# Optimization experiments

Measured on AMD Instinct MI355X. Metric: run time of the kernel, lower is better.

Reference implementation:

```python
import jax, jax.numpy as jnp
import numpy as np

D_MODEL = 2048
N_HEADS = 8
HEAD_DIM = D_MODEL // N_HEADS
SCALING = HEAD_DIM ** -0.5


def setup_inputs() -> dict:
    key = jax.random.key(0)
    ks = jax.random.split(key, 9)
    B, S, D = 2, 2048, D_MODEL
    std = D ** -0.5
    inp = {"x": jax.random.normal(ks[0], (B, S, D), dtype=jnp.float32)}
    names = ["Wq", "Wk", "Wv", "Wo"]
    for i, n in enumerate(names):
        inp[n] = jax.random.normal(ks[1 + i], (D, D), dtype=jnp.float32) * std
        inp["b" + n[1]] = jax.random.normal(ks[5 + i], (D,), dtype=jnp.float32) * 0.01
    return inp


def reference(x, Wq, bq, Wk, bk, Wv, bv, Wo, bo):
    B, S, D = x.shape
    H, hd = N_HEADS, HEAD_DIM

    def proj(W, b):
        # nn.Linear: x @ W.T + b, then split heads -> [B, H, S, hd]
        y = jnp.einsum("bsd,ed->bse", x, W) + b
        return y.reshape(B, S, H, hd).transpose(0, 2, 1, 3)

    q = proj(Wq, bq)
    k = proj(Wk, bk)
    v = proj(Wv, bv)

    # scaled QK^T: [B, H, S, S]
    attn_weights = jnp.einsum("bhqd,bhkd->bhqk", q, k) * SCALING
    causal = jnp.tril(jnp.ones((S, S), dtype=bool))  # [S, S]
    attn_weights = jnp.where(causal[None, None], attn_weights, -jnp.inf)
    attn_probs = jax.nn.softmax(attn_weights, axis=-1)

    out = jnp.einsum("bhqk,bhkd->bhqd", attn_probs, v)  # [B, H, S, hd]
    out = out.transpose(0, 2, 1, 3).reshape(B, S, D)
    out = jnp.einsum("bsd,ed->bse", out, Wo) + bo
    return (out, attn_probs)
```

## Files before the change

### kernel.cpp

```cpp
#include <hip/hip_runtime.h>
#include <cstdint>
#include <cstddef>

typedef _Float16 f16;
typedef __attribute__((ext_vector_type(4))) _Float16 f16x4;
typedef __attribute__((ext_vector_type(8))) _Float16 f16x8;
typedef __attribute__((ext_vector_type(4))) float f32x4;

#define NB 2
#define SEQ 2048
#define DM 2048
#define NH 8
#define HD 256
#define MT (NB * SEQ)

#define QSCALE 0.09016844f
#define CEXP   23.08312065f

__device__ __forceinline__ void gload16(const f16* g, f16* l) {
    __builtin_amdgcn_global_load_lds(
        (const __attribute__((address_space(1))) uint32_t*)(const void*)g,
        (__attribute__((address_space(3))) uint32_t*)(void*)l,
        16, 0, 0);
}

__global__ __launch_bounds__(256) void k_cvt5(
    const float* __restrict__ x, const float* __restrict__ Wq,
    const float* __restrict__ Wk, const float* __restrict__ Wv,
    const float* __restrict__ Wo,
    f16* __restrict__ xh, f16* __restrict__ Wqh, f16* __restrict__ Wkh,
    f16* __restrict__ Wvh, f16* __restrict__ Woh) {
    const int total = (MT * DM + 4 * DM * DM) / 4;
    for (int q = blockIdx.x * blockDim.x + threadIdx.x; q < total;
         q += gridDim.x * blockDim.x) {
        int i = q * 4;
        const float* src; f16* dst; int off;
        if (i < MT * DM) { src = x; dst = xh; off = i; }
        else {
            int j = i - MT * DM;
            int w = j >> 22;
            off = j & ((1 << 22) - 1);
            src = (w == 0) ? Wq : (w == 1) ? Wk : (w == 2) ? Wv : Wo;
            dst = (w == 0) ? Wqh : (w == 1) ? Wkh : (w == 2) ? Wvh : Woh;
        }
        f32x4 v = *(const f32x4*)(src + off);
        f16x4 h;
        h[0] = (f16)v[0]; h[1] = (f16)v[1]; h[2] = (f16)v[2]; h[3] = (f16)v[3];
        *(f16x4*)(dst + off) = h;
    }
}

__device__ __forceinline__ void stage3(const f16* __restrict__ A,
                                       const f16* __restrict__ B,
                                       int m0, int n0, int k0,
                                       f16* AL, f16* BL, int tid, int half) {
#pragma unroll
    for (int jj = 0; jj < 2; ++jj) {
        int j = half * 2 + jj;
        int flat = j * 4096 + tid * 8;
        int r = flat >> 6, c = flat & 63;
        int cs = c ^ ((r & 7) << 3);
        gload16(A + (size_t)(m0 + r) * DM + k0 + cs,
                AL + j * 4096 + (tid >> 6) * 512);
    }
    {
        int j = half;
        int flat = j * 4096 + tid * 8;
        int r = flat >> 6, c = flat & 63;
        int cs = c ^ ((r & 7) << 3);
        gload16(B + (size_t)(n0 + r) * DM + k0 + cs,
                BL + j * 4096 + (tid >> 6) * 512);
    }
}

__device__ __forceinline__ f16x8 rdfrag(const f16* buf, int rowbase, int lr,
                                        int lg, int kk) {
    int row = rowbase + lr;
    int c = (kk * 32 + lg * 8) ^ ((lr & 7) << 3);
    return *(const f16x8*)&buf[row * 64 + c];
}

__device__ __forceinline__ void gemm256x128_core(const f16* __restrict__ A,
                                                 const f16* __restrict__ B,
                                                 int m0, int n0,
                                                 f16* AL, f16* BL,
                                                 f32x4 acc[4][4]) {
    const int tid = threadIdx.x, wave = tid >> 6, lane = tid & 63;
    const int wm = wave >> 1, wn = wave & 1;
    const int lr = lane & 15, lg = lane >> 4;
    const int nt = DM / 64;

    stage3(A, B, m0, n0, 0, AL, BL, tid, 0);
    stage3(A, B, m0, n0, 0, AL, BL, tid, 1);
    stage3(A, B, m0, n0, 64, AL + 16384, BL + 8192, tid, 0);
    stage3(A, B, m0, n0, 64, AL + 16384, BL + 8192, tid, 1);
    asm volatile("s_waitcnt vmcnt(6)" ::: "memory");
    __builtin_amdgcn_s_barrier();
    __builtin_amdgcn_sched_barrier(0);

    for (int kt = 0; kt < nt; ++kt) {
        const f16* Ab = AL + (kt % 3) * 16384;
        const f16* Bb = BL + (kt % 3) * 8192;
        const int arb = wm * 64, brb = wn * 64;

#pragma unroll
        for (int ph = 0; ph < 2; ++ph) {
            f16x8 af[4], bf[4];
#pragma unroll
            for (int mf = 0; mf < 4; ++mf)
                af[mf] = rdfrag(Ab, arb + mf * 16, lr, lg, ph);
#pragma unroll
            for (int nf = 0; nf < 4; ++nf)
                bf[nf] = rdfrag(Bb, brb + nf * 16, lr, lg, ph);

            if (kt + 2 < nt)
                stage3(A, B, m0, n0, (kt + 2) * 64,
                       AL + ((kt + 2) % 3) * 16384,
                       BL + ((kt + 2) % 3) * 8192, tid, ph);

            __builtin_amdgcn_sched_barrier(0);
            if (ph == 1) {
                if (kt + 2 < nt)
                    asm volatile("s_waitcnt vmcnt(6)" ::: "memory");
                else if (kt + 1 < nt)
                    asm volatile("s_waitcnt vmcnt(0)" ::: "memory");
            }
            __builtin_amdgcn_s_barrier();
            asm volatile("s_waitcnt lgkmcnt(0)" ::: "memory");
            __builtin_amdgcn_sched_barrier(0);

            __builtin_amdgcn_s_setprio(1);
#pragma unroll
            for (int mi = 0; mi < 4; ++mi)
#pragma unroll
                for (int nj = 0; nj < 4; ++nj)
                    acc[mi][nj] = __builtin_amdgcn_mfma_f32_16x16x32_f16(
                        af[mi], bf[nj], acc[mi][nj], 0, 0, 0);
            __builtin_amdgcn_s_setprio(0);
            __builtin_amdgcn_s_barrier();
        }
    }
}

__global__ __launch_bounds__(512, 1) void k_proj_qkv(
    const f16* __restrict__ xh, const f16* __restrict__ Wq,
    const f16* __restrict__ Wk, const f16* __restrict__ Wv,
    const float* __restrict__ bq, const float* __restrict__ bk,
    const float* __restrict__ bv,
    f16* __restrict__ Qh, f16* __restrict__ Kh, f16* __restrict__ Vth) {
    __shared__ __align__(16) f16 AL[3 * 16384];
    __shared__ __align__(16) f16 BL[3 * 8192];
    const int mode = blockIdx.z;
    const f16* W = (mode == 0) ? Wq : (mode == 1) ? Wk : Wv;
    const float* bias = (mode == 0) ? bq : (mode == 1) ? bk : bv;

    const int phys = blockIdx.x + 16 * blockIdx.y;
    const int xcdq = phys & 7, idx = phys >> 3;
    const int m0 = (xcdq * 2 + (idx >> 4)) * 256;
    const int n0 = (idx & 15) * 128;

    f32x4 acc[4][4];
#pragma unroll
    for (int mi = 0; mi < 4; ++mi)
#pragma unroll
        for (int nj = 0; nj < 4; ++nj) acc[mi][nj] = (f32x4){0.f, 0.f, 0.f, 0.f};

    gemm256x128_core(xh, W, m0, n0, AL, BL, acc);

    const int lane = threadIdx.x & 63, wave = threadIdx.x >> 6;
    const int wm = wave >> 1, wn = wave & 1;
    const int lr = lane & 15, lg = lane >> 4;
#pragma unroll
    for (int nj = 0; nj < 4; ++nj) {
        int n = n0 + wn * 64 + nj * 16 + lr;
        float bb = bias[n];
        int h = n >> 8, d = n & 255;
#pragma unroll
        for (int mi = 0; mi < 4; ++mi) {
#pragma unroll
            for (int i = 0; i < 4; ++i) {
                int m = m0 + wm * 64 + mi * 16 + lg * 4 + i;
                int b = m >> 11, s = m & 2047;
                float v = acc[mi][nj][i] + bb;
                size_t bh = (size_t)(b * NH + h);
                if (mode == 0)
                    Qh[((bh * SEQ + s) << 8) + d] = (f16)(v * QSCALE);
                else if (mode == 1)
                    Kh[((bh * SEQ + s) << 8) + d] = (f16)v;
                else
                    Vth[((bh * HD + d) << 11) + s] = (f16)v;
            }
        }
    }
}

__global__ __launch_bounds__(512, 1) void k_proj_o(
    const f16* __restrict__ Oh, const f16* __restrict__ Wo,
    const float* __restrict__ bo, float* __restrict__ out) {
    __shared__ __align__(16) f16 AL[3 * 16384];
    __shared__ __align__(16) f16 BL[3 * 8192];

    const int phys = blockIdx.x + 16 * blockIdx.y;
    const int xcdq = phys & 7, idx = phys >> 3;
    const int m0 = (xcdq * 2 + (idx >> 4)) * 256;
    const int n0 = (idx & 15) * 128;

    f32x4 acc[4][4];
#pragma unroll
    for (int mi = 0; mi < 4; ++mi)
#pragma unroll
        for (int nj = 0; nj < 4; ++nj) acc[mi][nj] = (f32x4){0.f, 0.f, 0.f, 0.f};

    gemm256x128_core(Oh, Wo, m0, n0, AL, BL, acc);

    const int lane = threadIdx.x & 63, wave = threadIdx.x >> 6;
    const int wm = wave >> 1, wn = wave & 1;
    const int lr = lane & 15, lg = lane >> 4;
#pragma unroll
    for (int nj = 0; nj < 4; ++nj) {
        int n = n0 + wn * 64 + nj * 16 + lr;
        float bb = bo[n];
#pragma unroll
        for (int mi = 0; mi < 4; ++mi) {
#pragma unroll
            for (int i = 0; i < 4; ++i) {
                int m = m0 + wm * 64 + mi * 16 + lg * 4 + i;
                out[(size_t)m * DM + n] = acc[mi][nj][i] + bb;
            }
        }
    }
}

__device__ __forceinline__ void stageK(const f16* __restrict__ Kb, int kt,
                                       f16* buf, int wave, int lane) {
#pragma unroll
    for (int j = 0; j < 8; ++j) {
        int base = (j * 4 + wave) << 9;
        int flat = base + (lane << 3);
        int r = flat >> 8;
        int c = (flat & 255) ^ ((r & 7) << 3);
        gload16(Kb + (size_t)(kt * 64 + r) * HD + c, buf + base);
    }
}
__device__ __forceinline__ void stageV(const f16* __restrict__ Vb, int kt,
                                       f16* buf, int wave, int lane) {
#pragma unroll
    for (int j = 0; j < 8; ++j) {
        int base = (j * 4 + wave) << 9;
        int flat = base + (lane << 3);
        int rv = flat >> 6;
        int cv = (flat & 63) ^ ((rv & 3) << 3);
        gload16(Vb + ((size_t)rv << 11) + kt * 64 + cv, buf + base);
    }
}

__global__ __launch_bounds__(256, 2) void k_attn(
    const f16* __restrict__ Qh, const f16* __restrict__ Kh,
    const f16* __restrict__ Vth, float* __restrict__ P,
    f16* __restrict__ Oh) {
    __shared__ __align__(16) f16 B0[64 * 256];
    __shared__ __align__(16) f16 B1[64 * 256];
    __shared__ __align__(16) f16 Ps[4][16][72];

    const int bid = blockIdx.x;
    const int xcd = bid & 7;
    const int slot = bid >> 3;
    const int psel = slot >> 5;
    const int s5 = slot & 31;
    const int qb = psel ? s5 : (31 - s5);
    const int bhid = xcd * 2 + psel;
    const int b = bhid >> 3, h = bhid & 7;

    const int q0 = qb * 64;
    const int tid = threadIdx.x, wave = tid >> 6, lane = tid & 63;
    const int lr = lane & 15, lg = lane >> 4;
    const size_t bh = (size_t)bhid;
    const f16* Qb = Qh + (bh << 19);
    const f16* Kb = Kh + (bh << 19);
    const f16* Vb = Vth + (bh << 19);
    float* Pb = P + (bh << 22);

    const int kswz = (lr & 7) << 3;
    const int vswz = (lr & 3) << 3;

    f16x8 aq[8];
    {
        const f16* qrow = Qb + (size_t)(q0 + wave * 16 + lr) * HD + lg * 8;
#pragma unroll
        for (int kk = 0; kk < 8; ++kk) aq[kk] = *(const f16x8*)(qrow + kk * 32);
    }

    const int rowb = q0 + wave * 16 + lg * 4;
    const int nt = qb + 1;

    float psum[4] = {0.f, 0.f, 0.f, 0.f};

    stageK(Kb, 0, B0, wave, lane);
    for (int kt = 0; kt < nt; ++kt) {
        f16* cur = (kt & 1) ? B1 : B0;
        f16* nxt = (kt & 1) ? B0 : B1;
        if (kt + 1 < nt) {
            stageK(Kb, kt + 1, nxt, wave, lane);
            asm volatile("s_waitcnt vmcnt(8)" ::: "memory");
        } else {
            asm volatile("s_waitcnt vmcnt(0)" ::: "memory");
        }
        __builtin_amdgcn_s_barrier();
        __builtin_amdgcn_sched_barrier(0);

        f32x4 s[4];
#pragma unroll
        for (int nj = 0; nj < 4; ++nj) s[nj] = (f32x4){0.f, 0.f, 0.f, 0.f};
        __builtin_amdgcn_s_setprio(1);
#pragma unroll
        for (int kk = 0; kk < 8; ++kk) {
#pragma unroll
            for (int nj = 0; nj < 4; ++nj) {
                f16x8 bk = *(const f16x8*)&cur[(nj * 16 + lr) * 256 +
                                               ((kk * 32 + lg * 8) ^ kswz)];
                s[nj] = __builtin_amdgcn_mfma_f32_16x16x32_f16(aq[kk], bk, s[nj], 0, 0, 0);
            }
        }
        __builtin_amdgcn_s_setprio(0);
        const int colb = kt * 64 + lr;
#pragma unroll
        for (int i = 0; i < 4; ++i) {
            int row = rowb + i;
#pragma unroll
            for (int nj = 0; nj < 4; ++nj)
                psum[i] += (colb + nj * 16 <= row) ? exp2f(s[nj][i] - CEXP) : 0.f;
        }
        asm volatile("" ::: "memory");
        __builtin_amdgcn_s_barrier();
        __builtin_amdgcn_sched_barrier(0);
    }

    float inv[4];
#pragma unroll
    for (int i = 0; i < 4; ++i) {
        float l = psum[i];
        l += __shfl_xor(l, 1);
        l += __shfl_xor(l, 2);
        l += __shfl_xor(l, 4);
        l += __shfl_xor(l, 8);
        inv[i] = 1.f / l;
    }

    f32x4 o[16];
#pragma unroll
    for (int n = 0; n < 16; ++n) o[n] = (f32x4){0.f, 0.f, 0.f, 0.f};

    stageK(Kb, 0, B0, wave, lane);
    for (int kt = 0; kt < nt; ++kt) {
        stageV(Vb, kt, B1, wave, lane);
        if (kt == 0) asm volatile("s_waitcnt vmcnt(8)" ::: "memory");
        else         asm volatile("s_waitcnt vmcnt(10)" ::: "memory");
        __builtin_amdgcn_s_barrier();
        __builtin_amdgcn_sched_barrier(0);

        f32x4 s[4];
#pragma unroll
        for (int nj = 0; nj < 4; ++nj) s[nj] = (f32x4){0.f, 0.f, 0.f, 0.f};
        __builtin_amdgcn_s_setprio(1);
#pragma unroll
        for (int kk = 0; kk < 8; ++kk) {
#pragma unroll
            for (int nj = 0; nj < 4; ++nj) {
                f16x8 bk = *(const f16x8*)&B0[(nj * 16 + lr) * 256 +
                                              ((kk * 32 + lg * 8) ^ kswz)];
                s[nj] = __builtin_amdgcn_mfma_f32_16x16x32_f16(aq[kk], bk, s[nj], 0, 0, 0);
            }
        }
        __builtin_amdgcn_s_setprio(0);
#pragma unroll
        for (int i = 0; i < 4; ++i) {
            int row = rowb + i;
#pragma unroll
            for (int nj = 0; nj < 4; ++nj) {
                int col = kt * 64 + nj * 16 + lr;
                float pv = (col <= row) ? exp2f(s[nj][i] - CEXP) * inv[i] : 0.f;
                Ps[wave][lg * 4 + i][nj * 16 + lr] = (f16)pv;
            }
        }
        asm volatile("s_waitcnt vmcnt(0)" ::: "memory");
        __builtin_amdgcn_s_barrier();
        __builtin_amdgcn_sched_barrier(0);

        if (kt + 1 < nt) stageK(Kb, kt + 1, B0, wave, lane);

        __builtin_amdgcn_s_setprio(1);
#pragma unroll
        for (int kk2 = 0; kk2 < 2; ++kk2) {
            f16x8 pa = *(const f16x8*)&Ps[wave][lr][kk2 * 32 + lg * 8];
#pragma unroll
            for (int n = 0; n < 16; ++n) {
                f16x8 bv = *(const f16x8*)&B1[(n * 16 + lr) * 64 +
                                              ((kk2 * 32 + lg * 8) ^ vswz)];
                o[n] = __builtin_amdgcn_mfma_f32_16x16x32_f16(pa, bv, o[n], 0, 0, 0);
            }
        }
        __builtin_amdgcn_s_setprio(0);

#pragma unroll
        for (int h2 = 0; h2 < 2; ++h2) {
            int rr = h2 * 8 + (lane >> 3);
            int cc = (lane & 7) * 8;
            f16x8 ph = *(const f16x8*)&Ps[wave][rr][cc];
            int row = q0 + wave * 16 + rr;
            float* dst = Pb + (size_t)row * SEQ + kt * 64 + cc;
            f32x4 lo = {(float)ph[0], (float)ph[1], (float)ph[2], (float)ph[3]};
            f32x4 hi = {(float)ph[4], (float)ph[5], (float)ph[6], (float)ph[7]};
            *(f32x4*)dst = lo;
            *(f32x4*)(dst + 4) = hi;
        }

        asm volatile("" ::: "memory");
        __builtin_amdgcn_s_barrier();
        __builtin_amdgcn_sched_barrier(0);
    }

    int kstart = (qb + 1) * 64;
    if (kstart < SEQ) {
        f32x4 z = (f32x4){0.f, 0.f, 0.f, 0.f};
        for (int r = 0; r < 64; ++r) {
            float* rp = Pb + (size_t)(q0 + r) * SEQ;
            for (int c = kstart + tid * 4; c < SEQ; c += 1024)
                *(f32x4*)(rp + c) = z;
        }
    }

#pragma unroll
    for (int n = 0; n < 16; ++n) {
#pragma unroll
        for (int i = 0; i < 4; ++i) {
            int row = rowb + i;
            int d = n * 16 + lr;
            Oh[((size_t)b * SEQ + row) * DM + h * HD + d] = (f16)o[n][i];
        }
    }
}

extern "C" void kernel_launch(void* const* d_in, const int* in_sizes, int n_in,
                              void* d_out, int out_size, void* d_ws, size_t ws_size,
                              hipStream_t stream) {
    const float* x  = (const float*)d_in[0];
    const float* Wq = (const float*)d_in[1];
    const float* bq = (const float*)d_in[2];
    const float* Wk = (const float*)d_in[3];
    const float* bk = (const float*)d_in[4];
    const float* Wv = (const float*)d_in[5];
    const float* bv = (const float*)d_in[6];
    const float* Wo = (const float*)d_in[7];
    const float* bo = (const float*)d_in[8];

    float* out  = (float*)d_out;
    float* Pout = out + (size_t)MT * DM;

    f16* xh  = (f16*)Pout;
    f16* Wqh = xh + (size_t)MT * DM;
    f16* Wkh = Wqh + (size_t)DM * DM;
    f16* Wvh = Wkh + (size_t)DM * DM;

    f16* ws16 = (f16*)d_ws;
    f16* Woh = ws16;
    f16* Qh  = Woh + (size_t)DM * DM;
    f16* Kh  = Qh + (size_t)8388608;
    f16* Vth = Kh + (size_t)8388608;
    f16* Oh  = Vth + (size_t)8388608;
    if (ws_size < (size_t)(4194304 + 4 * 8388608) * sizeof(f16)) return;

    k_cvt5<<<2048, 256, 0, stream>>>(x, Wq, Wk, Wv, Wo, xh, Wqh, Wkh, Wvh, Woh);

    dim3 g1(DM / 128, MT / 256, 3);
    k_proj_qkv<<<g1, 512, 0, stream>>>(xh, Wqh, Wkh, Wvh, bq, bk, bv, Qh, Kh, Vth);

    k_attn<<<dim3(512), 256, 0, stream>>>(Qh, Kh, Vth, Pout, Oh);

    dim3 g3(DM / 128, MT / 256, 1);
    k_proj_o<<<g3, 512, 0, stream>>>(Oh, Woh, bo, out);
}
```

Measured before the change: 352.1 us.

## Use two waves per attention block, each computing 32 query rows

The attention kernel now runs 128 threads (2 waves) per block instead of 256, with each wave handling two 16-row query sub-tiles. Every K/V fragment read from LDS now feeds two MFMAs, which halves LDS read traffic per MFMA. The staging loops issue twice as many loads per wave, and the vmcnt thresholds are adjusted to match. Register use roughly doubles (the o accumulators go from 16 to 32 f32x4), the launch bounds drop to 1 block per SIMD set, and fewer waves are left to hide latency.

```diff
diff --git a/kernel.cpp b/kernel.cpp
--- a/kernel.cpp
+++ b/kernel.cpp
@@ -231,22 +231,22 @@
     }
 }
 
-__device__ __forceinline__ void stageK(const f16* __restrict__ Kb, int kt,
-                                       f16* buf, int wave, int lane) {
-#pragma unroll
-    for (int j = 0; j < 8; ++j) {
-        int base = (j * 4 + wave) << 9;
+__device__ __forceinline__ void stageK2(const f16* __restrict__ Kb, int kt,
+                                        f16* buf, int wave, int lane) {
+#pragma unroll
+    for (int j = 0; j < 16; ++j) {
+        int base = (j * 2 + wave) << 9;
         int flat = base + (lane << 3);
         int r = flat >> 8;
         int c = (flat & 255) ^ ((r & 7) << 3);
         gload16(Kb + (size_t)(kt * 64 + r) * HD + c, buf + base);
     }
 }
-__device__ __forceinline__ void stageV(const f16* __restrict__ Vb, int kt,
-                                       f16* buf, int wave, int lane) {
-#pragma unroll
-    for (int j = 0; j < 8; ++j) {
-        int base = (j * 4 + wave) << 9;
+__device__ __forceinline__ void stageV2(const f16* __restrict__ Vb, int kt,
+                                        f16* buf, int wave, int lane) {
+#pragma unroll
+    for (int j = 0; j < 16; ++j) {
+        int base = (j * 2 + wave) << 9;
         int flat = base + (lane << 3);
         int rv = flat >> 6;
         int cv = (flat & 63) ^ ((rv & 3) << 3);
@@ -254,13 +254,13 @@
     }
 }
 
-__global__ __launch_bounds__(256, 2) void k_attn(
+__global__ __launch_bounds__(128, 1) void k_attn(
     const f16* __restrict__ Qh, const f16* __restrict__ Kh,
     const f16* __restrict__ Vth, float* __restrict__ P,
     f16* __restrict__ Oh) {
     __shared__ __align__(16) f16 B0[64 * 256];
     __shared__ __align__(16) f16 B1[64 * 256];
-    __shared__ __align__(16) f16 Ps[4][16][72];
+    __shared__ __align__(16) f16 Ps[2][32][72];
 
     const int bid = blockIdx.x;
     const int xcd = bid & 7;
@@ -283,34 +283,41 @@
     const int kswz = (lr & 7) << 3;
     const int vswz = (lr & 3) << 3;
 
-    f16x8 aq[8];
-    {
-        const f16* qrow = Qb + (size_t)(q0 + wave * 16 + lr) * HD + lg * 8;
-#pragma unroll
-        for (int kk = 0; kk < 8; ++kk) aq[kk] = *(const f16x8*)(qrow + kk * 32);
-    }
-
-    const int rowb = q0 + wave * 16 + lg * 4;
+    f16x8 aq[2][8];
+#pragma unroll
+    for (int mi = 0; mi < 2; ++mi) {
+        const f16* qrow = Qb + (size_t)(q0 + wave * 32 + mi * 16 + lr) * HD + lg * 8;
+#pragma unroll
+        for (int kk = 0; kk < 8; ++kk) aq[mi][kk] = *(const f16x8*)(qrow + kk * 32);
+    }
+
+    const int rowb = q0 + wave * 32 + lg * 4;
     const int nt = qb + 1;
 
-    float psum[4] = {0.f, 0.f, 0.f, 0.f};
-
-    stageK(Kb, 0, B0, wave, lane);
+    float psum[2][4];
+#pragma unroll
+    for (int mi = 0; mi < 2; ++mi)
+#pragma unroll
+        for (int i = 0; i < 4; ++i) psum[mi][i] = 0.f;
+
+    stageK2(Kb, 0, B0, wave, lane);
     for (int kt = 0; kt < nt; ++kt) {
         f16* cur = (kt & 1) ? B1 : B0;
         f16* nxt = (kt & 1) ? B0 : B1;
         if (kt + 1 < nt) {
-            stageK(Kb, kt + 1, nxt, wave, lane);
-            asm volatile("s_waitcnt vmcnt(8)" ::: "memory");
+            stageK2(Kb, kt + 1, nxt, wave, lane);
+            asm volatile("s_waitcnt vmcnt(16)" ::: "memory");
         } else {
             asm volatile("s_waitcnt vmcnt(0)" ::: "memory");
         }
         __builtin_amdgcn_s_barrier();
         __builtin_amdgcn_sched_barrier(0);
 
-        f32x4 s[4];
-#pragma unroll
-        for (int nj = 0; nj < 4; ++nj) s[nj] = (f32x4){0.f, 0.f, 0.f, 0.f};
+        f32x4 s[2][4];
+#pragma unroll
+        for (int mi = 0; mi < 2; ++mi)
+#pragma unroll
+            for (int nj = 0; nj < 4; ++nj) s[mi][nj] = (f32x4){0.f, 0.f, 0.f, 0.f};
         __builtin_amdgcn_s_setprio(1);
 #pragma unroll
         for (int kk = 0; kk < 8; ++kk) {
@@ -318,49 +325,58 @@
             for (int nj = 0; nj < 4; ++nj) {
                 f16x8 bk = *(const f16x8*)&cur[(nj * 16 + lr) * 256 +
                                                ((kk * 32 + lg * 8) ^ kswz)];
-                s[nj] = __builtin_amdgcn_mfma_f32_16x16x32_f16(aq[kk], bk, s[nj], 0, 0, 0);
+                s[0][nj] = __builtin_amdgcn_mfma_f32_16x16x32_f16(aq[0][kk], bk, s[0][nj], 0, 0, 0);
+                s[1][nj] = __builtin_amdgcn_mfma_f32_16x16x32_f16(aq[1][kk], bk, s[1][nj], 0, 0, 0);
             }
         }
         __builtin_amdgcn_s_setprio(0);
         const int colb = kt * 64 + lr;
 #pragma unroll
-        for (int i = 0; i < 4; ++i) {
-            int row = rowb + i;
-#pragma unroll
-            for (int nj = 0; nj < 4; ++nj)
-                psum[i] += (colb + nj * 16 <= row) ? exp2f(s[nj][i] - CEXP) : 0.f;
-        }
+        for (int mi = 0; mi < 2; ++mi)
+#pragma unroll
+            for (int i = 0; i < 4; ++i) {
+                int row = rowb + mi * 16 + i;
+#pragma unroll
+                for (int nj = 0; nj < 4; ++nj)
+                    psum[mi][i] += (colb + nj * 16 <= row) ? exp2f(s[mi][nj][i] - CEXP) : 0.f;
+            }
         asm volatile("" ::: "memory");
         __builtin_amdgcn_s_barrier();
         __builtin_amdgcn_sched_barrier(0);
     }
 
-    float inv[4];
-#pragma unroll
-    for (int i = 0; i < 4; ++i) {
-        float l = psum[i];
-        l += __shfl_xor(l, 1);
-        l += __shfl_xor(l, 2);
-        l += __shfl_xor(l, 4);
-        l += __shfl_xor(l, 8);
-        inv[i] = 1.f / l;
-    }
-
-    f32x4 o[16];
-#pragma unroll
-    for (int n = 0; n < 16; ++n) o[n] = (f32x4){0.f, 0.f, 0.f, 0.f};
-
-    stageK(Kb, 0, B0, wave, lane);
+    float inv[2][4];
+#pragma unroll
+    for (int mi = 0; mi < 2; ++mi)
+#pragma unroll
+        for (int i = 0; i < 4; ++i) {
+            float l = psum[mi][i];
+            l += __shfl_xor(l, 1);
+            l += __shfl_xor(l, 2);
+            l += __shfl_xor(l, 4);
+            l += __shfl_xor(l, 8);
+            inv[mi][i] = 1.f / l;
+        }
+
+    f32x4 o[2][16];
+#pragma unroll
+    for (int mi = 0; mi < 2; ++mi)
+#pragma unroll
+        for (int n = 0; n < 16; ++n) o[mi][n] = (f32x4){0.f, 0.f, 0.f, 0.f};
+
+    stageK2(Kb, 0, B0, wave, lane);
     for (int kt = 0; kt < nt; ++kt) {
-        stageV(Vb, kt, B1, wave, lane);
-        if (kt == 0) asm volatile("s_waitcnt vmcnt(8)" ::: "memory");
-        else         asm volatile("s_waitcnt vmcnt(10)" ::: "memory");
+        stageV2(Vb, kt, B1, wave, lane);
+        if (kt == 0) asm volatile("s_waitcnt vmcnt(16)" ::: "memory");
+        else         asm volatile("s_waitcnt vmcnt(24)" ::: "memory");
         __builtin_amdgcn_s_barrier();
         __builtin_amdgcn_sched_barrier(0);
 
-        f32x4 s[4];
-#pragma unroll
-        for (int nj = 0; nj < 4; ++nj) s[nj] = (f32x4){0.f, 0.f, 0.f, 0.f};
+        f32x4 s[2][4];
+#pragma unroll
+        for (int mi = 0; mi < 2; ++mi)
+#pragma unroll
+            for (int nj = 0; nj < 4; ++nj) s[mi][nj] = (f32x4){0.f, 0.f, 0.f, 0.f};
         __builtin_amdgcn_s_setprio(1);
 #pragma unroll
         for (int kk = 0; kk < 8; ++kk) {
@@ -368,45 +384,50 @@
             for (int nj = 0; nj < 4; ++nj) {
                 f16x8 bk = *(const f16x8*)&B0[(nj * 16 + lr) * 256 +
                                               ((kk * 32 + lg * 8) ^ kswz)];
-                s[nj] = __builtin_amdgcn_mfma_f32_16x16x32_f16(aq[kk], bk, s[nj], 0, 0, 0);
+                s[0][nj] = __builtin_amdgcn_mfma_f32_16x16x32_f16(aq[0][kk], bk, s[0][nj], 0, 0, 0);
+                s[1][nj] = __builtin_amdgcn_mfma_f32_16x16x32_f16(aq[1][kk], bk, s[1][nj], 0, 0, 0);
             }
         }
         __builtin_amdgcn_s_setprio(0);
 #pragma unroll
-        for (int i = 0; i < 4; ++i) {
-            int row = rowb + i;
-#pragma unroll
-            for (int nj = 0; nj < 4; ++nj) {
-                int col = kt * 64 + nj * 16 + lr;
-                float pv = (col <= row) ? exp2f(s[nj][i] - CEXP) * inv[i] : 0.f;
-                Ps[wave][lg * 4 + i][nj * 16 + lr] = (f16)pv;
-            }
-        }
+        for (int mi = 0; mi < 2; ++mi)
+#pragma unroll
+            for (int i = 0; i < 4; ++i) {
+                int row = rowb + mi * 16 + i;
+#pragma unroll
+                for (int nj = 0; nj < 4; ++nj) {
+                    int col = kt * 64 + nj * 16 + lr;
+                    float pv = (col <= row) ? exp2f(s[mi][nj][i] - CEXP) * inv[mi][i] : 0.f;
+                    Ps[wave][mi * 16 + lg * 4 + i][nj * 16 + lr] = (f16)pv;
+                }
+            }
         asm volatile("s_waitcnt vmcnt(0)" ::: "memory");
         __builtin_amdgcn_s_barrier();
         __builtin_amdgcn_sched_barrier(0);
 
-        if (kt + 1 < nt) stageK(Kb, kt + 1, B0, wave, lane);
+        if (kt + 1 < nt) stageK2(Kb, kt + 1, B0, wave, lane);
 
         __builtin_amdgcn_s_setprio(1);
 #pragma unroll
         for (int kk2 = 0; kk2 < 2; ++kk2) {
-            f16x8 pa = *(const f16x8*)&Ps[wave][lr][kk2 * 32 + lg * 8];
+            f16x8 pa0 = *(const f16x8*)&Ps[wave][lr][kk2 * 32 + lg * 8];
+            f16x8 pa1 = *(const f16x8*)&Ps[wave][16 + lr][kk2 * 32 + lg * 8];
 #pragma unroll
             for (int n = 0; n < 16; ++n) {
                 f16x8 bv = *(const f16x8*)&B1[(n * 16 + lr) * 64 +
                                               ((kk2 * 32 + lg * 8) ^ vswz)];
-                o[n] = __builtin_amdgcn_mfma_f32_16x16x32_f16(pa, bv, o[n], 0, 0, 0);
+                o[0][n] = __builtin_amdgcn_mfma_f32_16x16x32_f16(pa0, bv, o[0][n], 0, 0, 0);
+                o[1][n] = __builtin_amdgcn_mfma_f32_16x16x32_f16(pa1, bv, o[1][n], 0, 0, 0);
             }
         }
         __builtin_amdgcn_s_setprio(0);
 
 #pragma unroll
-        for (int h2 = 0; h2 < 2; ++h2) {
+        for (int h2 = 0; h2 < 4; ++h2) {
             int rr = h2 * 8 + (lane >> 3);
             int cc = (lane & 7) * 8;
             f16x8 ph = *(const f16x8*)&Ps[wave][rr][cc];
-            int row = q0 + wave * 16 + rr;
+            int row = q0 + wave * 32 + rr;
             float* dst = Pb + (size_t)row * SEQ + kt * 64 + cc;
             f32x4 lo = {(float)ph[0], (float)ph[1], (float)ph[2], (float)ph[3]};
             f32x4 hi = {(float)ph[4], (float)ph[5], (float)ph[6], (float)ph[7]};
@@ -424,20 +445,22 @@
         f32x4 z = (f32x4){0.f, 0.f, 0.f, 0.f};
         for (int r = 0; r < 64; ++r) {
             float* rp = Pb + (size_t)(q0 + r) * SEQ;
-            for (int c = kstart + tid * 4; c < SEQ; c += 1024)
+            for (int c = kstart + tid * 4; c < SEQ; c += 512)
                 *(f32x4*)(rp + c) = z;
         }
     }
 
 #pragma unroll
-    for (int n = 0; n < 16; ++n) {
-#pragma unroll
-        for (int i = 0; i < 4; ++i) {
-            int row = rowb + i;
-            int d = n * 16 + lr;
-            Oh[((size_t)b * SEQ + row) * DM + h * HD + d] = (f16)o[n][i];
-        }
-    }
+    for (int mi = 0; mi < 2; ++mi)
+#pragma unroll
+        for (int n = 0; n < 16; ++n) {
+#pragma unroll
+            for (int i = 0; i < 4; ++i) {
+                int row = rowb + mi * 16 + i;
+                int d = n * 16 + lr;
+                Oh[((size_t)b * SEQ + row) * DM + h * HD + d] = (f16)o[mi][n][i];
+            }
+        }
 }
 
 extern "C" void kernel_launch(void* const* d_in, const int* in_sizes, int n_in,
@@ -474,7 +497,7 @@
     dim3 g1(DM / 128, MT / 256, 3);
     k_proj_qkv<<<g1, 512, 0, stream>>>(xh, Wqh, Wkh, Wvh, bq, bk, bv, Qh, Kh, Vth);
 
-    k_attn<<<dim3(512), 256, 0, stream>>>(Qh, Kh, Vth, Pout, Oh);
+    k_attn<<<dim3(512), 128, 0, stream>>>(Qh, Kh, Vth, Pout, Oh);
 
     dim3 g3(DM / 128, MT / 256, 1);
     k_proj_o<<<g3, 512, 0, stream>>>(Oh, Woh, bo, out);
```

After: 418.2 us. 18.8% more time.
